# Optimization experiments

Hardware: AMD Instinct MI355X
Metric: run time of the kernel (lower is better)

Reference implementation:

```python
import jax, jax.numpy as jnp
import numpy as np

N, D, E = 50000, 128, 800000
EPS = 1e-5


def setup_inputs() -> dict:
    key = jax.random.key(0)
    ks = jax.random.split(key, 16)
    x = jax.random.normal(ks[0], (N, D), dtype=jnp.float32)
    edge_index = jax.random.randint(ks[1], (2, E), 0, N, dtype=jnp.int32)
    s = 1.0 / np.sqrt(D)
    inp = {"x": x, "edge_index": edge_index}
    for i in range(3):
        inp[f"lng{i}"] = jnp.ones((D,), jnp.float32)
        inp[f"lnb{i}"] = jnp.zeros((D,), jnp.float32)
        inp[f"W{i}"] = jax.random.normal(ks[2 + 2 * i], (D, D), jnp.float32) * s
        inp[f"b{i}"] = jnp.zeros((D,), jnp.float32)
    return inp


def _gcn_norm(edge_index):
    # PyG GCNConv default: add self loops, symmetric normalization D^-1/2 (A+I) D^-1/2
    loop = jnp.arange(N, dtype=edge_index.dtype)
    src = jnp.concatenate([edge_index[0], loop])  # [E+N]
    dst = jnp.concatenate([edge_index[1], loop])
    deg = jax.ops.segment_sum(jnp.ones_like(dst, jnp.float32), dst, num_segments=N)
    dinv = jnp.where(deg > 0, jax.lax.rsqrt(jnp.maximum(deg, 1.0)), 0.0)
    norm = dinv[src] * dinv[dst]  # [E+N]
    return src, dst, norm


def _layer(h, g, bt, W, b, src, dst, norm):
    # LayerNorm -> ReLU -> GCNConv
    mu = jnp.mean(h, axis=-1, keepdims=True)
    var = jnp.mean(jnp.square(h - mu), axis=-1, keepdims=True)
    hn = (h - mu) * jax.lax.rsqrt(var + EPS) * g + bt
    hn = jax.nn.relu(hn) @ W  # [N, D]
    msg = norm[:, None] * hn[src]  # [E+N, D] gather
    return jax.ops.segment_sum(msg, dst, num_segments=N) + b


def reference(x, edge_index, lng0, lnb0, W0, b0, lng1, lnb1, W1, b1, lng2, lnb2, W2, b2):
    src, dst, norm = _gcn_norm(edge_index)
    # conv0 (GCNLayer) + residual
    x = _layer(x, lng0, lnb0, W0, b0, src, dst, norm) + x
    # conv1 (ResGCNLayer: two GCNLayers) + residual
    h = _layer(x, lng1, lnb1, W1, b1, src, dst, norm)
    h = _layer(h, lng2, lnb2, W2, b2, src, dst, norm)
    return h + x
```

## Files before the change

### kernel.cpp

```cpp
#include <hip/hip_runtime.h>

#define N_NODES 50000
#define DIM     128
#define E_EDGES 800000
#define ELLW    64

typedef __attribute__((ext_vector_type(8))) short short8;
typedef __attribute__((ext_vector_type(4))) float f32x4;

__device__ __forceinline__ float bflo(unsigned int u){ return __uint_as_float(u << 16); }
__device__ __forceinline__ float bfhi(unsigned int u){ return __uint_as_float(u & 0xFFFF0000u); }
__device__ __forceinline__ unsigned int f2bf(float f){
  unsigned int u = __float_as_uint(f);
  return (u + 0x7FFFu + ((u >> 16) & 1u)) >> 16;
}
__device__ __forceinline__ unsigned int pack2(float a, float b){
  return f2bf(a) | (f2bf(b) << 16);
}


__global__ __launch_bounds__(256) void count_kernel(const int* __restrict__ edges,
                                                    int* __restrict__ cnt){
  int e = blockIdx.x * 256 + threadIdx.x;
  if (e < E_EDGES) atomicAdd(&cnt[edges[E_EDGES + e]], 1);
}

__global__ __launch_bounds__(256) void dinv_kernel(const int* __restrict__ cnt,
                                                   float* __restrict__ dinv){
  int i = blockIdx.x * 256 + threadIdx.x;
  if (i < N_NODES) dinv[i] = rsqrtf((float)(cnt[i] + 1));
}

__global__ __launch_bounds__(256) void fill_kernel(const int* __restrict__ edges,
                                                   int* __restrict__ cur,
                                                   const float* __restrict__ dinv,
                                                   int2* __restrict__ ell){
  int e = blockIdx.x * 256 + threadIdx.x;
  if (e < E_EDGES){
    int s = edges[e];
    int d = edges[E_EDGES + e];
    int pos = atomicAdd(&cur[d], 1);
    int2 pk; pk.x = s; pk.y = __float_as_int(dinv[s] * dinv[d]);
    ell[(size_t)d * ELLW + pos] = pk;
  }
}

__global__ __launch_bounds__(256) void cvtw_all(const float* __restrict__ W0,
                                                const float* __restrict__ W1,
                                                const float* __restrict__ W2,
                                                unsigned short* __restrict__ Wt){
  int idx = blockIdx.x * 256 + threadIdx.x;
  int w = idx >> 14, r = idx & 16383;
  const float* W = (w == 0) ? W0 : (w == 1) ? W1 : W2;
  int k = r >> 7, n = r & 127;
  Wt[w * 16384 + n * 128 + k] = (unsigned short)f2bf(W[r]);
}


__global__ __launch_bounds__(256) void gemm_ln_mfma(const float* __restrict__ X,
                                                    const float* __restrict__ g,
                                                    const float* __restrict__ bt,
                                                    const unsigned short* __restrict__ Wt,
                                                    unsigned short* __restrict__ Y){
  __shared__ unsigned short ldsb[128 * 136];
  int tid = threadIdx.x;
  #pragma unroll
  for (int it = 0; it < 8; ++it){
    int c  = tid + it * 256;
    int n  = c >> 4, kc = c & 15;
    *(short8*)&ldsb[n * 136 + kc * 8] = *(const short8*)(Wt + n * 128 + kc * 8);
  }
  int wave = tid >> 6, lane = tid & 63, quad = lane >> 4, l15 = lane & 15;
  int rowbase = blockIdx.x * 128 + wave * 32;
  int rm0 = rowbase + l15;      if (rm0 > N_NODES - 1) rm0 = N_NODES - 1;
  int rm1 = rowbase + 16 + l15; if (rm1 > N_NODES - 1) rm1 = N_NODES - 1;

  float v0[4][8], v1[4][8];
  float s0 = 0.f, ss0 = 0.f, s1 = 0.f, ss1 = 0.f;
  #pragma unroll
  for (int kk = 0; kk < 4; ++kk){
    float4 xa = *(const float4*)(X + (size_t)rm0 * 128 + kk * 32 + quad * 8);
    float4 xb = *(const float4*)(X + (size_t)rm0 * 128 + kk * 32 + quad * 8 + 4);
    float4 ya = *(const float4*)(X + (size_t)rm1 * 128 + kk * 32 + quad * 8);
    float4 yb_ = *(const float4*)(X + (size_t)rm1 * 128 + kk * 32 + quad * 8 + 4);
    v0[kk][0]=xa.x; v0[kk][1]=xa.y; v0[kk][2]=xa.z; v0[kk][3]=xa.w;
    v0[kk][4]=xb.x; v0[kk][5]=xb.y; v0[kk][6]=xb.z; v0[kk][7]=xb.w;
    v1[kk][0]=ya.x; v1[kk][1]=ya.y; v1[kk][2]=ya.z; v1[kk][3]=ya.w;
    v1[kk][4]=yb_.x; v1[kk][5]=yb_.y; v1[kk][6]=yb_.z; v1[kk][7]=yb_.w;
    #pragma unroll
    for (int j = 0; j < 8; ++j){
      s0 += v0[kk][j]; ss0 += v0[kk][j] * v0[kk][j];
      s1 += v1[kk][j]; ss1 += v1[kk][j] * v1[kk][j];
    }
  }
  s0 += __shfl_xor(s0, 16, 64); ss0 += __shfl_xor(ss0, 16, 64);
  s0 += __shfl_xor(s0, 32, 64); ss0 += __shfl_xor(ss0, 32, 64);
  s1 += __shfl_xor(s1, 16, 64); ss1 += __shfl_xor(ss1, 16, 64);
  s1 += __shfl_xor(s1, 32, 64); ss1 += __shfl_xor(ss1, 32, 64);
  float mu0 = s0 * (1.0f/128.0f), var0 = ss0 * (1.0f/128.0f) - mu0*mu0;
  float mu1 = s1 * (1.0f/128.0f), var1 = ss1 * (1.0f/128.0f) - mu1*mu1;
  float rs0 = rsqrtf(var0 + 1e-5f), rs1 = rsqrtf(var1 + 1e-5f);

  short8 a0[4], a1[4];
  #pragma unroll
  for (int kk = 0; kk < 4; ++kk){
    float4 ga = *(const float4*)(g  + kk * 32 + quad * 8);
    float4 gb = *(const float4*)(g  + kk * 32 + quad * 8 + 4);
    float4 ba = *(const float4*)(bt + kk * 32 + quad * 8);
    float4 bb = *(const float4*)(bt + kk * 32 + quad * 8 + 4);
    float gg[8] = {ga.x,ga.y,ga.z,ga.w,gb.x,gb.y,gb.z,gb.w};
    float bbv[8] = {ba.x,ba.y,ba.z,ba.w,bb.x,bb.y,bb.z,bb.w};
    #pragma unroll
    for (int j = 0; j < 8; ++j){
      float h0 = fmaxf((v0[kk][j] - mu0) * rs0 * gg[j] + bbv[j], 0.0f);
      float h1 = fmaxf((v1[kk][j] - mu1) * rs1 * gg[j] + bbv[j], 0.0f);
      a0[kk][j] = (short)f2bf(h0);
      a1[kk][j] = (short)f2bf(h1);
    }
  }

  f32x4 acc[2][8];
  #pragma unroll
  for (int mt = 0; mt < 2; ++mt)
    #pragma unroll
    for (int nt = 0; nt < 8; ++nt) acc[mt][nt] = (f32x4){0.f, 0.f, 0.f, 0.f};
  __syncthreads();
  #pragma unroll
  for (int kk = 0; kk < 4; ++kk){
    #pragma unroll
    for (int nt = 0; nt < 8; ++nt){
      short8 b = *(const short8*)&ldsb[(nt * 16 + l15) * 136 + kk * 32 + quad * 8];
      acc[0][nt] = __builtin_amdgcn_mfma_f32_16x16x32_bf16(a0[kk], b, acc[0][nt], 0, 0, 0);
      acc[1][nt] = __builtin_amdgcn_mfma_f32_16x16x32_bf16(a1[kk], b, acc[1][nt], 0, 0, 0);
    }
  }
  #pragma unroll
  for (int mt = 0; mt < 2; ++mt)
    #pragma unroll
    for (int nt = 0; nt < 8; ++nt)
      #pragma unroll
      for (int r = 0; r < 4; ++r){
        int row = rowbase + mt * 16 + quad * 4 + r;
        if (row < N_NODES)
          Y[(size_t)row * 128 + nt * 16 + l15] = (unsigned short)f2bf(acc[mt][nt][r]);
      }
}


__global__ __launch_bounds__(256) void gemm_mfma(const unsigned short* __restrict__ A,
                                                 const unsigned short* __restrict__ Wt,
                                                 unsigned short* __restrict__ Y){
  __shared__ unsigned short ldsb[128 * 136];
  int tid = threadIdx.x;
  #pragma unroll
  for (int it = 0; it < 8; ++it){
    int c  = tid + it * 256;
    int n  = c >> 4, kc = c & 15;
    *(short8*)&ldsb[n * 136 + kc * 8] = *(const short8*)(Wt + n * 128 + kc * 8);
  }
  int wave = tid >> 6, lane = tid & 63, quad = lane >> 4, l15 = lane & 15;
  int rowbase = blockIdx.x * 128 + wave * 32;
  int rm0 = rowbase + l15;      if (rm0 > N_NODES - 1) rm0 = N_NODES - 1;
  int rm1 = rowbase + 16 + l15; if (rm1 > N_NODES - 1) rm1 = N_NODES - 1;

  short8 a0[4], a1[4];
  #pragma unroll
  for (int kk = 0; kk < 4; ++kk){
    a0[kk] = *(const short8*)(A + (size_t)rm0 * 128 + kk * 32 + quad * 8);
    a1[kk] = *(const short8*)(A + (size_t)rm1 * 128 + kk * 32 + quad * 8);
  }
  f32x4 acc[2][8];
  #pragma unroll
  for (int mt = 0; mt < 2; ++mt)
    #pragma unroll
    for (int nt = 0; nt < 8; ++nt) acc[mt][nt] = (f32x4){0.f, 0.f, 0.f, 0.f};
  __syncthreads();
  #pragma unroll
  for (int kk = 0; kk < 4; ++kk){
    #pragma unroll
    for (int nt = 0; nt < 8; ++nt){
      short8 b = *(const short8*)&ldsb[(nt * 16 + l15) * 136 + kk * 32 + quad * 8];
      acc[0][nt] = __builtin_amdgcn_mfma_f32_16x16x32_bf16(a0[kk], b, acc[0][nt], 0, 0, 0);
      acc[1][nt] = __builtin_amdgcn_mfma_f32_16x16x32_bf16(a1[kk], b, acc[1][nt], 0, 0, 0);
    }
  }
  #pragma unroll
  for (int mt = 0; mt < 2; ++mt)
    #pragma unroll
    for (int nt = 0; nt < 8; ++nt)
      #pragma unroll
      for (int r = 0; r < 4; ++r){
        int row = rowbase + mt * 16 + quad * 4 + r;
        if (row < N_NODES)
          Y[(size_t)row * 128 + nt * 16 + l15] = (unsigned short)f2bf(acc[mt][nt][r]);
      }
}


template<bool HAS_RES, bool DO_LN>
__global__ __launch_bounds__(256) void agg_kernel(const unsigned short* __restrict__ y,
                                                  const int* __restrict__ cnt,
                                                  const int2* __restrict__ ell,
                                                  const float* __restrict__ dinv,
                                                  const float* __restrict__ bias,
                                                  const float* __restrict__ res,
                                                  float* __restrict__ outp,
                                                  const float* __restrict__ lng,
                                                  const float* __restrict__ lnb,
                                                  unsigned short* __restrict__ hn_out){
  int pair = (blockIdx.x * 256 + threadIdx.x) >> 6;
  int lane = threadIdx.x & 63;
  int half = lane >> 5, hl = lane & 31;
  int node = pair * 2 + half;
  if (node >= N_NODES) return;
  const uint2* y2 = (const uint2*)y;

  float di = dinv[node];
  float ws = di * di;
  uint2 us = y2[(size_t)node * 32 + hl];
  float a0 = ws * bflo(us.x), a1 = ws * bfhi(us.x);
  float a2 = ws * bflo(us.y), a3 = ws * bfhi(us.y);

  int deg = cnt[node];
  int nb  = (deg + 3) >> 2;
  const int4* row = (const int4*)(ell + (size_t)node * ELLW);

  if (nb > 0){
    int4 ea0 = row[0], eb0 = row[1];
    uint2 g0 = y2[(size_t)ea0.x * 32 + hl];
    uint2 g1 = y2[(size_t)ea0.z * 32 + hl];
    uint2 g2 = y2[(size_t)eb0.x * 32 + hl];
    uint2 g3 = y2[(size_t)eb0.z * 32 + hl];
    for (int b = 1; b < nb; ++b){
      int4 ea1 = row[b * 2], eb1 = row[b * 2 + 1];
      uint2 h0 = y2[(size_t)ea1.x * 32 + hl];
      uint2 h1 = y2[(size_t)ea1.z * 32 + hl];
      uint2 h2 = y2[(size_t)eb1.x * 32 + hl];
      uint2 h3 = y2[(size_t)eb1.z * 32 + hl];
      float w0 = __int_as_float(ea0.y), w1 = __int_as_float(ea0.w);
      float w2 = __int_as_float(eb0.y), w3 = __int_as_float(eb0.w);
      a0 += w0*bflo(g0.x); a1 += w0*bfhi(g0.x); a2 += w0*bflo(g0.y); a3 += w0*bfhi(g0.y);
      a0 += w1*bflo(g1.x); a1 += w1*bfhi(g1.x); a2 += w1*bflo(g1.y); a3 += w1*bfhi(g1.y);
      a0 += w2*bflo(g2.x); a1 += w2*bfhi(g2.x); a2 += w2*bflo(g2.y); a3 += w2*bfhi(g2.y);
      a0 += w3*bflo(g3.x); a1 += w3*bfhi(g3.x); a2 += w3*bflo(g3.y); a3 += w3*bfhi(g3.y);
      ea0 = ea1; eb0 = eb1; g0 = h0; g1 = h1; g2 = h2; g3 = h3;
    }
    float w0 = __int_as_float(ea0.y), w1 = __int_as_float(ea0.w);
    float w2 = __int_as_float(eb0.y), w3 = __int_as_float(eb0.w);
    a0 += w0*bflo(g0.x); a1 += w0*bfhi(g0.x); a2 += w0*bflo(g0.y); a3 += w0*bfhi(g0.y);
    a0 += w1*bflo(g1.x); a1 += w1*bfhi(g1.x); a2 += w1*bflo(g1.y); a3 += w1*bfhi(g1.y);
    a0 += w2*bflo(g2.x); a1 += w2*bfhi(g2.x); a2 += w2*bflo(g2.y); a3 += w2*bfhi(g2.y);
    a0 += w3*bflo(g3.x); a1 += w3*bfhi(g3.x); a2 += w3*bflo(g3.y); a3 += w3*bfhi(g3.y);
  }

  float4 ub4 = ((const float4*)bias)[hl];
  a0 += ub4.x; a1 += ub4.y; a2 += ub4.z; a3 += ub4.w;
  if (HAS_RES){
    float4 ur = ((const float4*)res)[(size_t)node * 32 + hl];
    a0 += ur.x; a1 += ur.y; a2 += ur.z; a3 += ur.w;
  }
  if (outp){
    float4 o; o.x = a0; o.y = a1; o.z = a2; o.w = a3;
    ((float4*)outp)[(size_t)node * 32 + hl] = o;
  }

  if (DO_LN){
    float s = a0 + a1 + a2 + a3;
    float ss = a0*a0 + a1*a1 + a2*a2 + a3*a3;
    #pragma unroll
    for (int d = 16; d >= 1; d >>= 1){ s += __shfl_xor(s, d, 64); ss += __shfl_xor(ss, d, 64); }
    float mu  = s * (1.0f / 128.0f);
    float var = ss * (1.0f / 128.0f) - mu * mu;
    float rs  = rsqrtf(var + 1e-5f);
    float4 ug = ((const float4*)lng)[hl];
    float4 ubb = ((const float4*)lnb)[hl];
    float h0 = fmaxf((a0 - mu) * rs * ug.x + ubb.x, 0.0f);
    float h1 = fmaxf((a1 - mu) * rs * ug.y + ubb.y, 0.0f);
    float h2 = fmaxf((a2 - mu) * rs * ug.z + ubb.z, 0.0f);
    float h3 = fmaxf((a3 - mu) * rs * ug.w + ubb.w, 0.0f);
    uint2 ho; ho.x = pack2(h0, h1); ho.y = pack2(h2, h3);
    ((uint2*)hn_out)[(size_t)node * 32 + hl] = ho;
  }
}


extern "C" void kernel_launch(void* const* d_in, const int* in_sizes, int n_in,
                              void* d_out, int out_size, void* d_ws, size_t ws_size,
                              hipStream_t stream){
  const float* x    = (const float*)d_in[0];
  const int*   edges= (const int*)d_in[1];
  const float* lng0 = (const float*)d_in[2];
  const float* lnb0 = (const float*)d_in[3];
  const float* W0   = (const float*)d_in[4];
  const float* b0   = (const float*)d_in[5];
  const float* lng1 = (const float*)d_in[6];
  const float* lnb1 = (const float*)d_in[7];
  const float* W1   = (const float*)d_in[8];
  const float* b1   = (const float*)d_in[9];
  const float* lng2 = (const float*)d_in[10];
  const float* lnb2 = (const float*)d_in[11];
  const float* W2   = (const float*)d_in[12];
  const float* b2   = (const float*)d_in[13];

  char* p = (char*)d_ws;
  auto carve = [&](size_t bytes) -> void* {
    void* r = (void*)p;
    p += (bytes + 255) & ~(size_t)255;
    return r;
  };
  int*   cnt   = (int*)  carve(N_NODES * 4);
  int*   cur   = (int*)  carve(N_NODES * 4);
  int2*  ell   = (int2*) carve((size_t)N_NODES * ELLW * 8);
  size_t zspan = (char*)(ell + (size_t)N_NODES * ELLW) - (char*)cnt;
  float* dinv  = (float*)carve(N_NODES * 4);
  unsigned short* Wt = (unsigned short*)carve(3 * 128 * 128 * 2);
  unsigned short* hn = (unsigned short*)carve((size_t)N_NODES * 128 * 2);
  unsigned short* yb = (unsigned short*)carve((size_t)N_NODES * 128 * 2);
  float* out = (float*)d_out;

  hipMemsetAsync(cnt, 0, zspan, stream);

  count_kernel<<<(E_EDGES + 255) / 256, 256, 0, stream>>>(edges, cnt);
  dinv_kernel<<<(N_NODES + 255) / 256, 256, 0, stream>>>(cnt, dinv);
  fill_kernel<<<(E_EDGES + 255) / 256, 256, 0, stream>>>(edges, cur, dinv, ell);
  cvtw_all<<<192, 256, 0, stream>>>(W0, W1, W2, Wt);

  const int GEMM_GRID = (N_NODES + 127) / 128;
  const int PAIR_GRID = (N_NODES / 2 + 3) / 4;

  gemm_ln_mfma<<<GEMM_GRID, 256, 0, stream>>>(x, lng0, lnb0, Wt, yb);
  agg_kernel<true, true><<<PAIR_GRID, 256, 0, stream>>>(yb, cnt, ell, dinv,
                                                        b0, x, out, lng1, lnb1, hn);
  gemm_mfma<<<GEMM_GRID, 256, 0, stream>>>(hn, Wt + 16384, yb);
  agg_kernel<false, true><<<PAIR_GRID, 256, 0, stream>>>(yb, cnt, ell, dinv,
                                                         b1, nullptr, nullptr, lng2, lnb2, hn);
  gemm_mfma<<<GEMM_GRID, 256, 0, stream>>>(hn, Wt + 32768, yb);
  agg_kernel<true, false><<<PAIR_GRID, 256, 0, stream>>>(yb, cnt, ell, dinv,
                                                         b2, out, out, nullptr, nullptr, nullptr);
}
```

Baseline: 327.5 us.

## Aggregate four nodes per wave with cooperative ELL loads and shuffles

The aggregation kernel now maps 16 lanes to each node, four nodes per wave, with 16-byte feature gathers. Each lane loads part of the node's ELL row once, and neighbour indices and weights are broadcast by wave shuffles instead of per-lane int4 row loads. The loop runs to the maximum degree of the four nodes, so low-degree nodes sit idle while their neighbours finish. Preprocessing records each edge's slot during the count pass, which removes the second atomic pass and the dinv kernel and array, and computes rsqrt on the fly.

```diff
diff --git a/kernel.cpp b/kernel.cpp
--- a/kernel.cpp
+++ b/kernel.cpp
@@ -20,28 +20,26 @@
 
 
 __global__ __launch_bounds__(256) void count_kernel(const int* __restrict__ edges,
-                                                    int* __restrict__ cnt){
+                                                    int* __restrict__ cnt,
+                                                    int* __restrict__ epos){
   int e = blockIdx.x * 256 + threadIdx.x;
-  if (e < E_EDGES) atomicAdd(&cnt[edges[E_EDGES + e]], 1);
-}
-
-__global__ __launch_bounds__(256) void dinv_kernel(const int* __restrict__ cnt,
-                                                   float* __restrict__ dinv){
-  int i = blockIdx.x * 256 + threadIdx.x;
-  if (i < N_NODES) dinv[i] = rsqrtf((float)(cnt[i] + 1));
+  if (e < E_EDGES) epos[e] = atomicAdd(&cnt[edges[E_EDGES + e]], 1);
 }
 
 __global__ __launch_bounds__(256) void fill_kernel(const int* __restrict__ edges,
-                                                   int* __restrict__ cur,
-                                                   const float* __restrict__ dinv,
+                                                   const int* __restrict__ epos,
+                                                   const int* __restrict__ cnt,
                                                    int2* __restrict__ ell){
   int e = blockIdx.x * 256 + threadIdx.x;
   if (e < E_EDGES){
     int s = edges[e];
     int d = edges[E_EDGES + e];
-    int pos = atomicAdd(&cur[d], 1);
-    int2 pk; pk.x = s; pk.y = __float_as_int(dinv[s] * dinv[d]);
-    ell[(size_t)d * ELLW + pos] = pk;
+    int pos = epos[e];
+    if (pos < ELLW){
+      float w = rsqrtf((float)(cnt[s] + 1)) * rsqrtf((float)(cnt[d] + 1));
+      int2 pk; pk.x = s; pk.y = __float_as_int(w);
+      ell[(size_t)d * ELLW + pos] = pk;
+    }
   }
 }
 
@@ -201,85 +199,108 @@
 __global__ __launch_bounds__(256) void agg_kernel(const unsigned short* __restrict__ y,
                                                   const int* __restrict__ cnt,
                                                   const int2* __restrict__ ell,
-                                                  const float* __restrict__ dinv,
                                                   const float* __restrict__ bias,
                                                   const float* __restrict__ res,
                                                   float* __restrict__ outp,
                                                   const float* __restrict__ lng,
                                                   const float* __restrict__ lnb,
                                                   unsigned short* __restrict__ hn_out){
-  int pair = (blockIdx.x * 256 + threadIdx.x) >> 6;
+  int wv   = (blockIdx.x * 256 + threadIdx.x) >> 6;
   int lane = threadIdx.x & 63;
-  int half = lane >> 5, hl = lane & 31;
-  int node = pair * 2 + half;
-  if (node >= N_NODES) return;
-  const uint2* y2 = (const uint2*)y;
-
-  float di = dinv[node];
+  int hl   = lane & 15;
+  int node = wv * 4 + (lane >> 4);
+  int selbase = lane & 48;
+  const uint4* y4 = (const uint4*)y;
+
+  int deg = cnt[node];
+  float di = rsqrtf((float)(deg + 1));
   float ws = di * di;
-  uint2 us = y2[(size_t)node * 32 + hl];
-  float a0 = ws * bflo(us.x), a1 = ws * bfhi(us.x);
-  float a2 = ws * bflo(us.y), a3 = ws * bfhi(us.y);
-
-  int deg = cnt[node];
-  int nb  = (deg + 3) >> 2;
-  const int4* row = (const int4*)(ell + (size_t)node * ELLW);
-
-  if (nb > 0){
-    int4 ea0 = row[0], eb0 = row[1];
-    uint2 g0 = y2[(size_t)ea0.x * 32 + hl];
-    uint2 g1 = y2[(size_t)ea0.z * 32 + hl];
-    uint2 g2 = y2[(size_t)eb0.x * 32 + hl];
-    uint2 g3 = y2[(size_t)eb0.z * 32 + hl];
-    for (int b = 1; b < nb; ++b){
-      int4 ea1 = row[b * 2], eb1 = row[b * 2 + 1];
-      uint2 h0 = y2[(size_t)ea1.x * 32 + hl];
-      uint2 h1 = y2[(size_t)ea1.z * 32 + hl];
-      uint2 h2 = y2[(size_t)eb1.x * 32 + hl];
-      uint2 h3 = y2[(size_t)eb1.z * 32 + hl];
-      float w0 = __int_as_float(ea0.y), w1 = __int_as_float(ea0.w);
-      float w2 = __int_as_float(eb0.y), w3 = __int_as_float(eb0.w);
-      a0 += w0*bflo(g0.x); a1 += w0*bfhi(g0.x); a2 += w0*bflo(g0.y); a3 += w0*bfhi(g0.y);
-      a0 += w1*bflo(g1.x); a1 += w1*bfhi(g1.x); a2 += w1*bflo(g1.y); a3 += w1*bfhi(g1.y);
-      a0 += w2*bflo(g2.x); a1 += w2*bfhi(g2.x); a2 += w2*bflo(g2.y); a3 += w2*bfhi(g2.y);
-      a0 += w3*bflo(g3.x); a1 += w3*bfhi(g3.x); a2 += w3*bflo(g3.y); a3 += w3*bfhi(g3.y);
-      ea0 = ea1; eb0 = eb1; g0 = h0; g1 = h1; g2 = h2; g3 = h3;
-    }
-    float w0 = __int_as_float(ea0.y), w1 = __int_as_float(ea0.w);
-    float w2 = __int_as_float(eb0.y), w3 = __int_as_float(eb0.w);
-    a0 += w0*bflo(g0.x); a1 += w0*bfhi(g0.x); a2 += w0*bflo(g0.y); a3 += w0*bfhi(g0.y);
-    a0 += w1*bflo(g1.x); a1 += w1*bfhi(g1.x); a2 += w1*bflo(g1.y); a3 += w1*bfhi(g1.y);
-    a0 += w2*bflo(g2.x); a1 += w2*bfhi(g2.x); a2 += w2*bflo(g2.y); a3 += w2*bfhi(g2.y);
-    a0 += w3*bflo(g3.x); a1 += w3*bfhi(g3.x); a2 += w3*bflo(g3.y); a3 += w3*bfhi(g3.y);
-  }
-
-  float4 ub4 = ((const float4*)bias)[hl];
-  a0 += ub4.x; a1 += ub4.y; a2 += ub4.z; a3 += ub4.w;
+
+  const int2* row = ell + (size_t)node * ELLW;
+  int2 e0 = row[hl], e1 = row[hl + 16], e2 = row[hl + 32], e3 = row[hl + 48];
+
+  int J = deg;
+  J = max(J, __shfl_xor(J, 16, 64));
+  J = max(J, __shfl_xor(J, 32, 64));
+
+  uint4 us = y4[(size_t)node * 16 + hl];
+  float acc0 = ws * bflo(us.x), acc1 = ws * bfhi(us.x);
+  float acc2 = ws * bflo(us.y), acc3 = ws * bfhi(us.y);
+  float acc4 = ws * bflo(us.z), acc5 = ws * bfhi(us.z);
+  float acc6 = ws * bflo(us.w), acc7 = ws * bfhi(us.w);
+
+  auto block16 = [&](int2 ee, int base16){
+    int rem = J - base16;
+    if (rem <= 0) return;
+    int nch = (min(rem, 16) + 3) >> 2;
+    for (int c = 0; c < nch; ++c){
+      int rb = c * 4;
+      int sA = __shfl(ee.x, selbase | (rb + 0), 64);
+      int sB = __shfl(ee.x, selbase | (rb + 1), 64);
+      int sC = __shfl(ee.x, selbase | (rb + 2), 64);
+      int sD = __shfl(ee.x, selbase | (rb + 3), 64);
+      float wA = __uint_as_float((unsigned)__shfl(ee.y, selbase | (rb + 0), 64));
+      float wB = __uint_as_float((unsigned)__shfl(ee.y, selbase | (rb + 1), 64));
+      float wC = __uint_as_float((unsigned)__shfl(ee.y, selbase | (rb + 2), 64));
+      float wD = __uint_as_float((unsigned)__shfl(ee.y, selbase | (rb + 3), 64));
+      uint4 gA = y4[(size_t)sA * 16 + hl];
+      uint4 gB = y4[(size_t)sB * 16 + hl];
+      uint4 gC = y4[(size_t)sC * 16 + hl];
+      uint4 gD = y4[(size_t)sD * 16 + hl];
+      acc0 += wA*bflo(gA.x); acc1 += wA*bfhi(gA.x); acc2 += wA*bflo(gA.y); acc3 += wA*bfhi(gA.y);
+      acc4 += wA*bflo(gA.z); acc5 += wA*bfhi(gA.z); acc6 += wA*bflo(gA.w); acc7 += wA*bfhi(gA.w);
+      acc0 += wB*bflo(gB.x); acc1 += wB*bfhi(gB.x); acc2 += wB*bflo(gB.y); acc3 += wB*bfhi(gB.y);
+      acc4 += wB*bflo(gB.z); acc5 += wB*bfhi(gB.z); acc6 += wB*bflo(gB.w); acc7 += wB*bfhi(gB.w);
+      acc0 += wC*bflo(gC.x); acc1 += wC*bfhi(gC.x); acc2 += wC*bflo(gC.y); acc3 += wC*bfhi(gC.y);
+      acc4 += wC*bflo(gC.z); acc5 += wC*bfhi(gC.z); acc6 += wC*bflo(gC.w); acc7 += wC*bfhi(gC.w);
+      acc0 += wD*bflo(gD.x); acc1 += wD*bfhi(gD.x); acc2 += wD*bflo(gD.y); acc3 += wD*bfhi(gD.y);
+      acc4 += wD*bflo(gD.z); acc5 += wD*bfhi(gD.z); acc6 += wD*bflo(gD.w); acc7 += wD*bfhi(gD.w);
+    }
+  };
+  block16(e0, 0); block16(e1, 16); block16(e2, 32); block16(e3, 48);
+
+  float4 ubA = ((const float4*)bias)[hl * 2];
+  float4 ubB = ((const float4*)bias)[hl * 2 + 1];
+  acc0 += ubA.x; acc1 += ubA.y; acc2 += ubA.z; acc3 += ubA.w;
+  acc4 += ubB.x; acc5 += ubB.y; acc6 += ubB.z; acc7 += ubB.w;
   if (HAS_RES){
-    float4 ur = ((const float4*)res)[(size_t)node * 32 + hl];
-    a0 += ur.x; a1 += ur.y; a2 += ur.z; a3 += ur.w;
+    float4 urA = ((const float4*)res)[(size_t)node * 32 + hl * 2];
+    float4 urB = ((const float4*)res)[(size_t)node * 32 + hl * 2 + 1];
+    acc0 += urA.x; acc1 += urA.y; acc2 += urA.z; acc3 += urA.w;
+    acc4 += urB.x; acc5 += urB.y; acc6 += urB.z; acc7 += urB.w;
   }
   if (outp){
-    float4 o; o.x = a0; o.y = a1; o.z = a2; o.w = a3;
-    ((float4*)outp)[(size_t)node * 32 + hl] = o;
+    float4 oA; oA.x = acc0; oA.y = acc1; oA.z = acc2; oA.w = acc3;
+    float4 oB; oB.x = acc4; oB.y = acc5; oB.z = acc6; oB.w = acc7;
+    ((float4*)outp)[(size_t)node * 32 + hl * 2]     = oA;
+    ((float4*)outp)[(size_t)node * 32 + hl * 2 + 1] = oB;
   }
 
   if (DO_LN){
-    float s = a0 + a1 + a2 + a3;
-    float ss = a0*a0 + a1*a1 + a2*a2 + a3*a3;
-    #pragma unroll
-    for (int d = 16; d >= 1; d >>= 1){ s += __shfl_xor(s, d, 64); ss += __shfl_xor(ss, d, 64); }
+    float s  = acc0 + acc1 + acc2 + acc3 + acc4 + acc5 + acc6 + acc7;
+    float ss = acc0*acc0 + acc1*acc1 + acc2*acc2 + acc3*acc3
+             + acc4*acc4 + acc5*acc5 + acc6*acc6 + acc7*acc7;
+    #pragma unroll
+    for (int d = 8; d >= 1; d >>= 1){ s += __shfl_xor(s, d, 64); ss += __shfl_xor(ss, d, 64); }
     float mu  = s * (1.0f / 128.0f);
     float var = ss * (1.0f / 128.0f) - mu * mu;
     float rs  = rsqrtf(var + 1e-5f);
-    float4 ug = ((const float4*)lng)[hl];
-    float4 ubb = ((const float4*)lnb)[hl];
-    float h0 = fmaxf((a0 - mu) * rs * ug.x + ubb.x, 0.0f);
-    float h1 = fmaxf((a1 - mu) * rs * ug.y + ubb.y, 0.0f);
-    float h2 = fmaxf((a2 - mu) * rs * ug.z + ubb.z, 0.0f);
-    float h3 = fmaxf((a3 - mu) * rs * ug.w + ubb.w, 0.0f);
-    uint2 ho; ho.x = pack2(h0, h1); ho.y = pack2(h2, h3);
-    ((uint2*)hn_out)[(size_t)node * 32 + hl] = ho;
+    float4 ugA = ((const float4*)lng)[hl * 2];
+    float4 ugB = ((const float4*)lng)[hl * 2 + 1];
+    float4 ubbA = ((const float4*)lnb)[hl * 2];
+    float4 ubbB = ((const float4*)lnb)[hl * 2 + 1];
+    float h0 = fmaxf((acc0 - mu) * rs * ugA.x + ubbA.x, 0.0f);
+    float h1 = fmaxf((acc1 - mu) * rs * ugA.y + ubbA.y, 0.0f);
+    float h2 = fmaxf((acc2 - mu) * rs * ugA.z + ubbA.z, 0.0f);
+    float h3 = fmaxf((acc3 - mu) * rs * ugA.w + ubbA.w, 0.0f);
+    float h4 = fmaxf((acc4 - mu) * rs * ugB.x + ubbB.x, 0.0f);
+    float h5 = fmaxf((acc5 - mu) * rs * ugB.y + ubbB.y, 0.0f);
+    float h6 = fmaxf((acc6 - mu) * rs * ugB.z + ubbB.z, 0.0f);
+    float h7 = fmaxf((acc7 - mu) * rs * ugB.w + ubbB.w, 0.0f);
+    uint4 ho;
+    ho.x = pack2(h0, h1); ho.y = pack2(h2, h3);
+    ho.z = pack2(h4, h5); ho.w = pack2(h6, h7);
+    ((uint4*)hn_out)[(size_t)node * 16 + hl] = ho;
   }
 }
 
@@ -309,10 +330,9 @@
     return r;
   };
   int*   cnt   = (int*)  carve(N_NODES * 4);
-  int*   cur   = (int*)  carve(N_NODES * 4);
   int2*  ell   = (int2*) carve((size_t)N_NODES * ELLW * 8);
   size_t zspan = (char*)(ell + (size_t)N_NODES * ELLW) - (char*)cnt;
-  float* dinv  = (float*)carve(N_NODES * 4);
+  int*   epos  = (int*)  carve((size_t)E_EDGES * 4);
   unsigned short* Wt = (unsigned short*)carve(3 * 128 * 128 * 2);
   unsigned short* hn = (unsigned short*)carve((size_t)N_NODES * 128 * 2);
   unsigned short* yb = (unsigned short*)carve((size_t)N_NODES * 128 * 2);
@@ -320,21 +340,20 @@
 
   hipMemsetAsync(cnt, 0, zspan, stream);
 
-  count_kernel<<<(E_EDGES + 255) / 256, 256, 0, stream>>>(edges, cnt);
-  dinv_kernel<<<(N_NODES + 255) / 256, 256, 0, stream>>>(cnt, dinv);
-  fill_kernel<<<(E_EDGES + 255) / 256, 256, 0, stream>>>(edges, cur, dinv, ell);
+  count_kernel<<<(E_EDGES + 255) / 256, 256, 0, stream>>>(edges, cnt, epos);
+  fill_kernel<<<(E_EDGES + 255) / 256, 256, 0, stream>>>(edges, epos, cnt, ell);
   cvtw_all<<<192, 256, 0, stream>>>(W0, W1, W2, Wt);
 
   const int GEMM_GRID = (N_NODES + 127) / 128;
-  const int PAIR_GRID = (N_NODES / 2 + 3) / 4;
+  const int AGG_GRID  = N_NODES / 4 / 4;
 
   gemm_ln_mfma<<<GEMM_GRID, 256, 0, stream>>>(x, lng0, lnb0, Wt, yb);
-  agg_kernel<true, true><<<PAIR_GRID, 256, 0, stream>>>(yb, cnt, ell, dinv,
-                                                        b0, x, out, lng1, lnb1, hn);
+  agg_kernel<true, true><<<AGG_GRID, 256, 0, stream>>>(yb, cnt, ell,
+                                                       b0, x, out, lng1, lnb1, hn);
   gemm_mfma<<<GEMM_GRID, 256, 0, stream>>>(hn, Wt + 16384, yb);
-  agg_kernel<false, true><<<PAIR_GRID, 256, 0, stream>>>(yb, cnt, ell, dinv,
-                                                         b1, nullptr, nullptr, lng2, lnb2, hn);
+  agg_kernel<false, true><<<AGG_GRID, 256, 0, stream>>>(yb, cnt, ell,
+                                                        b1, nullptr, nullptr, lng2, lnb2, hn);
   gemm_mfma<<<GEMM_GRID, 256, 0, stream>>>(hn, Wt + 32768, yb);
-  agg_kernel<true, false><<<PAIR_GRID, 256, 0, stream>>>(yb, cnt, ell, dinv,
-                                                         b2, out, out, nullptr, nullptr, nullptr);
-}
+  agg_kernel<true, false><<<AGG_GRID, 256, 0, stream>>>(yb, cnt, ell,
+                                                        b2, out, out, nullptr, nullptr, nullptr);
+}
```

Result: faster. 300.3 us (-8.3%).
